# Optimization experiments

Hardware: AMD Instinct MI355X
Metric: run time of the kernel (lower is better)

The kernel has to match this reference:

```python
import jax, jax.numpy as jnp
import numpy as np

N_COARSE = 262145   # GMGN self.n
K_LEVELS = 5        # self.k
M_NBR = 9           # self.m
HID = 2048          # hidden_channels


def _build_grid():
    # replicates GMGN.init_toep_kernel (mtype='toep_mg')
    n_fine = 2 * (N_COARSE - 1) + 1          # 524289
    x = np.linspace(-1.0, 1.0, n_fine)
    x_lst, idx_lst = [], []
    for _ in range(K_LEVELS):
        n = x.shape[0]
        idx = np.arange((n - 1) // 2 - M_NBR + 1, (n - 1) // 2 + M_NBR)[1::2]  # m-1 center pts
        idx_lst.append(idx)
        x_lst.append(x[idx])
        x = x[::2]                            # injection1d
    x_lst.append(x)                           # coarse grid
    xs = np.concatenate(x_lst)[:, None].astype(np.float32)   # (N_eval, 1)
    nbrs = np.stack(idx_lst[::-1]).astype(np.int64)          # (k, m-1), coarse->fine
    return xs, nbrs


def setup_inputs() -> dict:
    key = jax.random.key(0)
    xs_np, nbrs_np = _build_grid()
    dims = [1, HID, HID, HID, HID, 1]
    inp = {"xs": jnp.asarray(xs_np), "nbrs": jnp.asarray(nbrs_np), "k": K_LEVELS, "m": M_NBR}
    ks = jax.random.split(key, 10)
    for j in range(5):
        bd = 1.0 / np.sqrt(dims[j])           # nn.Linear default init range
        inp[f"w{j}"] = jax.random.uniform(ks[2 * j], (dims[j], dims[j + 1]), jnp.float32, -bd, bd)
        inp[f"b{j}"] = jax.random.uniform(ks[2 * j + 1], (dims[j + 1],), jnp.float32, -bd, bd)
    return inp


def _interp1d(a):
    # linear prolongation: (n,) -> (2n-1,); even slots copy, odd slots average
    out = jnp.zeros((2 * a.shape[0] - 1,), a.dtype)
    out = out.at[0::2].set(a)
    return out.at[1::2].set(0.5 * (a[:-1] + a[1:]))


def _forward(xs, Ws, bs, nbrs, k, m):
    h = xs
    for W, b in zip(Ws, bs):
        h = jax.nn.relu(h @ W + b)            # MLP appends relu after every Linear (incl. last)
    Amg = h[:, 0]                             # (N_eval,) pointwise kernel values
    band = m - 1
    Abands = [Amg[band * i: band * (i + 1)] for i in range(k)][::-1]
    Ah = Amg[band * k:]                       # coarse kernel, length (n0-1)/2^k + 1
    for i in range(k):
        Ah = _interp1d(Ah)                    # upsample one level
        Ah = Ah.at[nbrs[i]].set(Abands[i])    # overwrite center band with exact MLP evals
    return Ah[None, None]                     # (1, 1, 2*(n-1)+1)


def reference(xs, w0, b0, w1, b1, w2, b2, w3, b3, w4, b4, nbrs, k, m):
    return _forward(xs, (w0, w1, w2, w3, w4), (b0, b1, b2, b3, b4), nbrs, k, m)
```

## Files before the change

kernel.cpp:

```cpp
#include <hip/hip_runtime.h>
#include <stdint.h>

#define HID    2048
#define MPTS   16425
#define MTILES 129
#define NTIL   16
#define KTIL   64
#define BIMG   5120

typedef float    f32x4 __attribute__((ext_vector_type(4)));
typedef _Float16 f16x8 __attribute__((ext_vector_type(8)));


__global__ void pack_w16(const float* __restrict__ w1,
                         const float* __restrict__ w2,
                         const float* __restrict__ w3,
                         _Float16* __restrict__ wp) {
    const int kt = blockIdx.x, nt = blockIdx.y, L = blockIdx.z;
    const float* W = (L == 0) ? w1 : ((L == 1) ? w2 : w3);
    __shared__ float tl[128 * 33];
    const int tid = threadIdx.x;
    const int k  = tid >> 3;
    const int nc = (tid & 7) * 16;
    const float* src = W + (size_t)(kt * 32 + k) * HID + nt * 128 + nc;
    #pragma unroll
    for (int j = 0; j < 16; ++j) tl[(nc + j) * 33 + k] = src[j];
    __syncthreads();
    const size_t base = (size_t)(L * 1024 + nt * 64 + kt) * BIMG;
    for (int e = tid; e < BIMG; e += 256) {
        int n = e / 40, kk = e - n * 40;
        wp[base + e] = (kk < 32) ? (_Float16)tl[n * 33 + kk] : (_Float16)0.f;
    }
}

__global__ void layer0p(const float* __restrict__ xs,
                        const float* __restrict__ w0,
                        const float* __restrict__ b0,
                        _Float16* __restrict__ Ahg,
                        _Float16* __restrict__ Alg, int row0) {
    const int r = blockIdx.x;
    const int grow = row0 + r;
    const int j0 = threadIdx.x * 8;
    const float x = (grow < MPTS) ? xs[grow] : 0.f;
    f16x8 h, l;
    #pragma unroll
    for (int q = 0; q < 8; ++q) {
        float v = x * w0[j0 + q] + b0[j0 + q];
        v = v > 0.f ? v : 0.f;
        _Float16 hs = (_Float16)v;
        h[q] = hs;
        l[q] = (_Float16)(v - (float)hs);
    }
    const int t = r >> 7, rowgrp = (r >> 4) & 7, lidx = r & 15;
    const int kt = j0 >> 5, quad = (j0 >> 3) & 3;
    const size_t dst = ((size_t)(t * 64 + kt) << 12) + rowgrp * 512 + quad * 128 + lidx * 8;
    *(f16x8*)(Ahg + dst) = h;
    *(f16x8*)(Alg + dst) = l;
}

__launch_bounds__(256, 3)
__global__ void gemm_hl(const _Float16* __restrict__ Ahg,
                        const _Float16* __restrict__ Alg,
                        const _Float16* __restrict__ wp,
                        const float* __restrict__ bias,
                        _Float16* __restrict__ Chg,
                        _Float16* __restrict__ Clg,
                        int layer, int write_lo) {
    __shared__ _Float16 Bs[4][BIMG];

    const int tid  = threadIdx.x;
    const int lane = tid & 63;
    const int wave = tid >> 6;
    const int quad = lane >> 4;
    const int lidx = lane & 15;

    const int nwg = (int)(gridDim.x * gridDim.y);
    const int L   = (int)(blockIdx.y * gridDim.x + blockIdx.x);
    const int F   = (L & 7) * (nwg >> 3) + (L >> 3);
    const int nt  = F & 15;
    const int mt  = F >> 4;

    const int mbase = (wave >> 1) * 64;
    const int nbase = (wave & 1) * 64;

    const char* gW = (const char*)(wp + (size_t)(layer * 1024 + nt * 64) * BIMG);

    const size_t abase = ((size_t)(mt * 64) << 12) + (size_t)(mbase >> 4) * 512 + (size_t)lane * 8;
    const _Float16* aH = Ahg + abase;
    const _Float16* aL = Alg + abase;

    f32x4 acc[4][4];
    #pragma unroll
    for (int i = 0; i < 4; ++i)
        #pragma unroll
        for (int j = 0; j < 4; ++j) acc[i][j] = (f32x4)0.f;

#define PF_B(KT, BUF) do {                                                            \
    const char* nW_ = gW + (size_t)(KT) * (BIMG * 2);                                 \
    char* dW_ = (char*)&Bs[BUF][0];                                                   \
    for (int t = wave; t < 10; t += 4) {                                              \
        __builtin_amdgcn_global_load_lds(                                             \
            (const __attribute__((address_space(1))) unsigned int*)(nW_ + t * 1024 + lane * 16), \
            (__attribute__((address_space(3))) unsigned int*)(dW_ + t * 1024), 16, 0, 0); \
    }                                                                                 \
} while (0)

#define LD_A(KT, H, Lo) do {                                                          \
    const size_t ak_ = (size_t)(KT) << 12;                                            \
    _Pragma("unroll")                                                                 \
    for (int mm = 0; mm < 4; ++mm) {                                                  \
        H[mm]  = *(const f16x8*)(aH + ak_ + mm * 512);                                \
        Lo[mm] = *(const f16x8*)(aL + ak_ + mm * 512);                                \
    }                                                                                 \
} while (0)

#define LD_B(BUF, BF) do {                                                            \
    _Pragma("unroll")                                                                 \
    for (int nn = 0; nn < 4; ++nn) {                                                  \
        int r_ = nbase + nn * 16 + lidx;                                              \
        BF[nn] = *(const f16x8*)(&Bs[BUF][r_ * 40 + quad * 8]);                       \
    }                                                                                 \
} while (0)

#define MFMA32(AH, AL, BF) do {                                                       \
    _Pragma("unroll")                                                                 \
    for (int mm = 0; mm < 4; ++mm)                                                    \
        _Pragma("unroll")                                                             \
        for (int nn = 0; nn < 4; ++nn) {                                              \
            acc[mm][nn] = __builtin_amdgcn_mfma_f32_16x16x32_f16(AH[mm], BF[nn], acc[mm][nn], 0, 0, 0); \
            acc[mm][nn] = __builtin_amdgcn_mfma_f32_16x16x32_f16(AL[mm], BF[nn], acc[mm][nn], 0, 0, 0); \
        }                                                                             \
} while (0)

#define SUPER(S, P, DO_PF, DO_A2) do {                                                \
    f16x8 bfr0_[4];                                                                   \
    LD_B(2 * (P), bfr0_);                                                             \
    if (DO_PF) { PF_B(2 * (S) + 2, 2 * ((P) ^ 1)); PF_B(2 * (S) + 3, 2 * ((P) ^ 1) + 1); } \
    LD_A(2 * (S) + 1, nah, nal);                                                      \
    MFMA32(cah, cal, bfr0_);                                                          \
    f16x8 bfr1_[4];                                                                   \
    LD_B(2 * (P) + 1, bfr1_);                                                         \
    if (DO_A2) LD_A(2 * (S) + 2, cah, cal);                                           \
    MFMA32(nah, nal, bfr1_);                                                          \
    __syncthreads();                                                                  \
} while (0)

    f16x8 cah[4], cal[4], nah[4], nal[4];

    PF_B(0, 0);
    PF_B(1, 1);
    LD_A(0, cah, cal);
    __syncthreads();

    for (int ss = 0; ss < 15; ++ss) {
        SUPER(2 * ss,     0, 1, 1);
        SUPER(2 * ss + 1, 1, 1, 1);
    }
    SUPER(30, 0, 1, 1);
    SUPER(31, 1, 0, 0);

#undef SUPER
#undef MFMA32
#undef LD_B
#undef LD_A
#undef PF_B

    #pragma unroll
    for (int nn = 0; nn < 4; ++nn) {
        const int col = nt * 128 + nbase + nn * 16 + lidx;
        const float bv = bias[col];
        const int kt2 = col >> 5, quad2 = (col >> 3) & 3, j2 = col & 7;
        const size_t cb = ((size_t)(mt * 64 + kt2) << 12) + quad2 * 128 + j2;
        #pragma unroll
        for (int mm = 0; mm < 4; ++mm) {
            const int rowg = (mbase >> 4) + mm;
            #pragma unroll
            for (int r = 0; r < 4; ++r) {
                const int lidx2 = quad * 4 + r;
                float v = acc[mm][nn][r] + bv;
                v = v > 0.f ? v : 0.f;
                _Float16 hs = (_Float16)v;
                const size_t idx = cb + rowg * 512 + lidx2 * 8;
                Chg[idx] = hs;
                if (write_lo) Clg[idx] = (_Float16)(v - (float)hs);
            }
        }
    }
}

__global__ void layer4p(const _Float16* __restrict__ Ahg,
                        const float* __restrict__ w4,
                        const float* __restrict__ b4,
                        float* __restrict__ Amg, int row0) {
    __shared__ float ps[256];
    const int mt = blockIdx.x;
    const int t = threadIdx.x;
    const int row = t & 127, half = t >> 7;
    const int rowgrp = row >> 4, lidx = row & 15;
    const size_t base = ((size_t)(mt * 64) << 12) + rowgrp * 512 + lidx * 8;
    float s = 0.f;
    for (int kt = half * 32; kt < half * 32 + 32; ++kt) {
        const _Float16* ph = Ahg + base + ((size_t)kt << 12);
        const float* wv = w4 + kt * 32;
        #pragma unroll
        for (int quad = 0; quad < 4; ++quad) {
            f16x8 hv = *(const f16x8*)(ph + quad * 128);
            #pragma unroll
            for (int j = 0; j < 8; ++j)
                s += (float)hv[j] * wv[quad * 8 + j];
        }
    }
    ps[t] = s;
    __syncthreads();
    if (t < 128) {
        const int grow = row0 + mt * 128 + t;
        if (grow < MPTS) {
            float v = ps[t] + ps[t + 128] + b4[0];
            Amg[grow] = v > 0.f ? v : 0.f;
        }
    }
}

__global__ void layer0f(const float* __restrict__ xs, const float* __restrict__ w0,
                        const float* __restrict__ b0, float* __restrict__ A, int row0) {
    const int r = blockIdx.x;
    const int j = threadIdx.x * 8;
    const float x = (row0 + r < MPTS) ? xs[row0 + r] : 0.f;
    float* out = A + (size_t)r * HID + j;
    #pragma unroll
    for (int q = 0; q < 8; ++q) {
        float v = x * w0[j + q] + b0[j + q];
        out[q] = v > 0.f ? v : 0.f;
    }
}

__launch_bounds__(256)
__global__ void gemm_valu(const float* __restrict__ A, const float* __restrict__ W,
                          const float* __restrict__ bias, float* __restrict__ C) {
    __shared__ float As[16][132];
    __shared__ float Ws[16][132];
    const int tid = threadIdx.x;
    const int tx = tid & 15, ty = tid >> 4;
    const int n0 = blockIdx.x * 128;
    const int m0 = blockIdx.y * 128;
    const int am = tid & 127, ak = (tid >> 7) * 8;
    const int wn = (tid & 15) * 8, wk = tid >> 4;
    const float* aptr = A + (size_t)(m0 + am) * HID + ak;
    const float* wptr = W + (size_t)wk * HID + n0 + wn;
    float acc[8][8];
    #pragma unroll
    for (int i = 0; i < 8; ++i)
        #pragma unroll
        for (int j = 0; j < 8; ++j) acc[i][j] = 0.f;
    for (int k0 = 0; k0 < HID; k0 += 16) {
        f32x4 a0 = *(const f32x4*)(aptr + k0);
        f32x4 a1 = *(const f32x4*)(aptr + k0 + 4);
        f32x4 w0v = *(const f32x4*)(wptr + (size_t)k0 * HID);
        f32x4 w1v = *(const f32x4*)(wptr + (size_t)k0 * HID + 4);
        __syncthreads();
        As[ak + 0][am] = a0[0]; As[ak + 1][am] = a0[1];
        As[ak + 2][am] = a0[2]; As[ak + 3][am] = a0[3];
        As[ak + 4][am] = a1[0]; As[ak + 5][am] = a1[1];
        As[ak + 6][am] = a1[2]; As[ak + 7][am] = a1[3];
        *(f32x4*)&Ws[wk][wn]     = w0v;
        *(f32x4*)&Ws[wk][wn + 4] = w1v;
        __syncthreads();
        #pragma unroll
        for (int kk = 0; kk < 16; ++kk) {
            f32x4 av0 = *(const f32x4*)&As[kk][ty * 8];
            f32x4 av1 = *(const f32x4*)&As[kk][ty * 8 + 4];
            f32x4 bv0 = *(const f32x4*)&Ws[kk][tx * 8];
            f32x4 bv1 = *(const f32x4*)&Ws[kk][tx * 8 + 4];
            float a[8] = {av0[0], av0[1], av0[2], av0[3], av1[0], av1[1], av1[2], av1[3]};
            float b[8] = {bv0[0], bv0[1], bv0[2], bv0[3], bv1[0], bv1[1], bv1[2], bv1[3]};
            #pragma unroll
            for (int i = 0; i < 8; ++i)
                #pragma unroll
                for (int j = 0; j < 8; ++j) acc[i][j] += a[i] * b[j];
        }
    }
    #pragma unroll
    for (int i = 0; i < 8; ++i) {
        const int m = m0 + ty * 8 + i;
        #pragma unroll
        for (int jc = 0; jc < 2; ++jc) {
            const int n = n0 + tx * 8 + jc * 4;
            f32x4 v4;
            #pragma unroll
            for (int q = 0; q < 4; ++q) {
                float v = acc[i][jc * 4 + q] + bias[n + q];
                v4[q] = v > 0.f ? v : 0.f;
            }
            *(f32x4*)(C + (size_t)m * HID + n) = v4;
        }
    }
}

__global__ void layer4f(const float* __restrict__ A, const float* __restrict__ w4,
                        const float* __restrict__ b4, float* __restrict__ Amg, int row0) {
    const int lane = threadIdx.x & 63;
    const int wave = threadIdx.x >> 6;
    const int r    = blockIdx.x * 4 + wave;
    if (row0 + r >= MPTS) return;
    const float* ap = A + (size_t)r * HID;
    float s = 0.f;
    #pragma unroll
    for (int c = 0; c < 8; ++c) {
        const int col = c * 256 + lane * 4;
        f32x4 av = *(const f32x4*)(ap + col);
        f32x4 wv = *(const f32x4*)(w4 + col);
        s += av[0] * wv[0] + av[1] * wv[1] + av[2] * wv[2] + av[3] * wv[3];
    }
    #pragma unroll
    for (int off = 32; off; off >>= 1) s += __shfl_down(s, off);
    if (lane == 0) {
        float v = s + b4[0];
        Amg[row0 + r] = v > 0.f ? v : 0.f;
    }
}

__global__ void mg_level(const float* __restrict__ in, float* __restrict__ outf,
                         const int* __restrict__ nbrs_base, int level,
                         const float* __restrict__ band, int n_out) {
    const int j = blockIdx.x * 256 + threadIdx.x;
    if (j >= n_out) return;
    float v;
    if (j & 1) v = 0.5f * (in[j >> 1] + in[(j >> 1) + 1]);
    else       v = in[j >> 1];
    const int stride =
        (nbrs_base[1] == 0 && nbrs_base[3] == 0 && nbrs_base[5] == 0) ? 2 : 1;
    #pragma unroll
    for (int t = 0; t < 8; ++t) {
        const int idx = nbrs_base[(level * 8 + t) * stride];
        if (j == idx) v = band[t];
    }
    outf[j] = v;
}

extern "C" void kernel_launch(void* const* d_in, const int* in_sizes, int n_in,
                              void* d_out, int out_size, void* d_ws, size_t ws_size,
                              hipStream_t stream) {
    int iXS=0, iNB=1, iW0=4, iB0=5, iW1=6, iB1=7, iW2=8, iB2=9,
        iW3=10, iB3=11, iW4=12, iB4=13;
    if (n_in >= 14) {
        if (in_sizes[0] == HID) {
            iB0=0; iB1=1; iB2=2; iB3=3; iB4=4; iNB=7;
            iW0=8; iW1=9; iW2=10; iW3=11; iW4=12; iXS=13;
        } else if (!(in_sizes[1] == 40 || in_sizes[1] == 80)) {
            iXS=0; iW0=1; iB0=2; iW1=3; iB1=4; iW2=5; iB2=6;
            iW3=7; iB3=8; iW4=9; iB4=10; iNB=11;
        }
    }
    const float* xs = (const float*)d_in[iXS];
    const int* nbrs = (const int*)d_in[iNB];
    const float* w0 = (const float*)d_in[iW0];
    const float* b0 = (const float*)d_in[iB0];
    const float* w1 = (const float*)d_in[iW1];
    const float* b1 = (const float*)d_in[iB1];
    const float* w2 = (const float*)d_in[iW2];
    const float* b2 = (const float*)d_in[iB2];
    const float* w3 = (const float*)d_in[iW3];
    const float* b3 = (const float*)d_in[iB3];
    const float* w4 = (const float*)d_in[iW4];
    const float* b4 = (const float*)d_in[iB4];

    char* ws = (char*)d_ws;
    const size_t szAmg = 66048;
    const size_t szAh1 = 524544;
    const size_t szAh2 = 1048832;
    float* Amg = (float*)(ws);
    float* ahA = (float*)(ws + szAmg);
    float* ahB = (float*)(ws + szAmg + szAh1);
    const size_t casc_end = szAmg + szAh1 + szAh2;
    const size_t szW    = (size_t)3 * 1024 * BIMG * 2;
    const size_t per_tile = 2ull * 128 * HID * 4;

    const int use_mfma = (ws_size >= casc_end + szW + per_tile) ? 1 : 0;

    _Float16* wp = (_Float16*)(ws + casc_end);
    const size_t buf_start = use_mfma ? (casc_end + szW) : casc_end;

    size_t avail = ws_size - buf_start;
    int CT = (int)(avail / per_tile);
    if (CT < 1) CT = 1;
    if (CT > 96) CT = 96;

    if (use_mfma) {
        const size_t half = (size_t)CT * 128 * HID;
        _Float16* bAh = (_Float16*)(ws + buf_start);
        _Float16* bAl = bAh + half;
        _Float16* bBh = bAh + 2 * half;
        _Float16* bBl = bAh + 3 * half;

        pack_w16<<<dim3(KTIL, NTIL, 3), 256, 0, stream>>>(w1, w2, w3, wp);

        for (int t0 = 0; t0 < MTILES; t0 += CT) {
            int tiles = (MTILES - t0 < CT) ? (MTILES - t0) : CT;
            int row0 = t0 * 128;
            layer0p<<<dim3(tiles * 128), 256, 0, stream>>>(xs, w0, b0, bAh, bAl, row0);
            dim3 ggrid(NTIL, tiles);
            gemm_hl<<<ggrid, 256, 0, stream>>>(bAh, bAl, wp, b1, bBh, bBl, 0, 1);
            gemm_hl<<<ggrid, 256, 0, stream>>>(bBh, bBl, wp, b2, bAh, bAl, 1, 1);
            gemm_hl<<<ggrid, 256, 0, stream>>>(bAh, bAl, wp, b3, bBh, bBl, 2, 0);
            layer4p<<<dim3(tiles), 256, 0, stream>>>(bBh, w4, b4, Amg, row0);
        }
    } else {
        float* bufA = (float*)(ws + buf_start);
        float* bufB = (float*)(ws + buf_start + (size_t)CT * 128 * HID * 4);
        for (int t0 = 0; t0 < MTILES; t0 += CT) {
            int tiles = (MTILES - t0 < CT) ? (MTILES - t0) : CT;
            int row0 = t0 * 128;
            layer0f<<<dim3(tiles * 128), 256, 0, stream>>>(xs, w0, b0, bufA, row0);
            dim3 ggrid(NTIL, tiles);
            gemm_valu<<<ggrid, 256, 0, stream>>>(bufA, w1, b1, bufB);
            gemm_valu<<<ggrid, 256, 0, stream>>>(bufB, w2, b2, bufA);
            gemm_valu<<<ggrid, 256, 0, stream>>>(bufA, w3, b3, bufB);
            layer4f<<<dim3(tiles * 32), 256, 0, stream>>>(bufB, w4, b4, Amg, row0);
        }
    }

    const float* cur = Amg + 40;
    float* dsts[5] = {ahA, ahB, ahA, ahB, (float*)d_out};
    int n = 16385;
    for (int i = 0; i < 5; ++i) {
        int n_out = 2 * n - 1;
        mg_level<<<dim3((n_out + 255) / 256), 256, 0, stream>>>(
            cur, dsts[i], nbrs, i, Amg + 8 * (4 - i), n_out);
        cur = dsts[i];
        n = n_out;
    }
    (void)out_size;
}
```

Baseline: 1.031 ms.

## Restructure GEMM k-loop into 4-slot ring with vmcnt-gated barriers

Replaces the double-buffered super-iteration loop of the hi/lo fp16 MFMA GEMM with a four-slot LDS ring that prefetches B three k-tiles ahead via global_load_lds. Each step waits only on a counted vmcnt before a raw s_barrier, rather than a full __syncthreads after every pair of tiles. MFMA sections run at raised wave priority. This aims for deeper latency hiding and fewer full drains, at the cost of more LDS per block (which may lower occupancy) and fragile hand-tuned wait counts. Each wave now issues 3 fixed 1 KB chunks, so B reads run past the 10 KB tile; the weight buffer is padded to cover the overrun.

```diff
diff --git a/kernel.cpp b/kernel.cpp
--- a/kernel.cpp
+++ b/kernel.cpp
@@ -7,6 +7,7 @@
 #define NTIL   16
 #define KTIL   64
 #define BIMG   5120
+#define BSLOT  6144
 
 typedef float    f32x4 __attribute__((ext_vector_type(4)));
 typedef _Float16 f16x8 __attribute__((ext_vector_type(8)));
@@ -66,7 +67,7 @@
                         _Float16* __restrict__ Chg,
                         _Float16* __restrict__ Clg,
                         int layer, int write_lo) {
-    __shared__ _Float16 Bs[4][BIMG];
+    __shared__ _Float16 Bs[4][BSLOT];
 
     const int tid  = threadIdx.x;
     const int lane = tid & 63;
@@ -98,10 +99,12 @@
 #define PF_B(KT, BUF) do {                                                            \
     const char* nW_ = gW + (size_t)(KT) * (BIMG * 2);                                 \
     char* dW_ = (char*)&Bs[BUF][0];                                                   \
-    for (int t = wave; t < 10; t += 4) {                                              \
+    const int t0_ = wave * 3;                                                         \
+    _Pragma("unroll")                                                                 \
+    for (int c_ = 0; c_ < 3; ++c_) {                                                  \
         __builtin_amdgcn_global_load_lds(                                             \
-            (const __attribute__((address_space(1))) unsigned int*)(nW_ + t * 1024 + lane * 16), \
-            (__attribute__((address_space(3))) unsigned int*)(dW_ + t * 1024), 16, 0, 0); \
+            (const __attribute__((address_space(1))) unsigned int*)(nW_ + (t0_ + c_) * 1024 + lane * 16), \
+            (__attribute__((address_space(3))) unsigned int*)(dW_ + (t0_ + c_) * 1024), 16, 0, 0); \
     }                                                                                 \
 } while (0)
 
@@ -132,34 +135,48 @@
         }                                                                             \
 } while (0)
 
-#define SUPER(S, P, DO_PF, DO_A2) do {                                                \
-    f16x8 bfr0_[4];                                                                   \
-    LD_B(2 * (P), bfr0_);                                                             \
-    if (DO_PF) { PF_B(2 * (S) + 2, 2 * ((P) ^ 1)); PF_B(2 * (S) + 3, 2 * ((P) ^ 1) + 1); } \
-    LD_A(2 * (S) + 1, nah, nal);                                                      \
-    MFMA32(cah, cal, bfr0_);                                                          \
-    f16x8 bfr1_[4];                                                                   \
-    LD_B(2 * (P) + 1, bfr1_);                                                         \
-    if (DO_A2) LD_A(2 * (S) + 2, cah, cal);                                           \
-    MFMA32(nah, nal, bfr1_);                                                          \
-    __syncthreads();                                                                  \
+#define GATE(N) do {                                                                  \
+    asm volatile("s_waitcnt vmcnt(%0)" :: "n"(N));                                    \
+    __builtin_amdgcn_sched_barrier(0);                                                \
+    __builtin_amdgcn_s_barrier();                                                     \
+    __builtin_amdgcn_sched_barrier(0);                                                \
+} while (0)
+
+#define BODY(KT, BUF, GN, DO_PF, DO_A, CH, CL, NH, NL) do {                           \
+    GATE(GN);                                                                         \
+    f16x8 bfr_[4];                                                                    \
+    LD_B(BUF, bfr_);                                                                  \
+    if (DO_A)  LD_A((KT) + 1, NH, NL);                                                \
+    if (DO_PF) PF_B((KT) + 3, ((KT) + 3) & 3);                                        \
+    __builtin_amdgcn_s_setprio(1);                                                    \
+    MFMA32(CH, CL, bfr_);                                                             \
+    __builtin_amdgcn_s_setprio(0);                                                    \
 } while (0)
 
     f16x8 cah[4], cal[4], nah[4], nal[4];
 
+    LD_A(0, cah, cal);
     PF_B(0, 0);
     PF_B(1, 1);
-    LD_A(0, cah, cal);
-    __syncthreads();
-
-    for (int ss = 0; ss < 15; ++ss) {
-        SUPER(2 * ss,     0, 1, 1);
-        SUPER(2 * ss + 1, 1, 1, 1);
-    }
-    SUPER(30, 0, 1, 1);
-    SUPER(31, 1, 0, 0);
-
-#undef SUPER
+    PF_B(2, 2);
+
+    BODY(0, 0,  6, 1, 1, cah, cal, nah, nal);
+    BODY(1, 1, 14, 1, 1, nah, nal, cah, cal);
+    BODY(2, 2, 22, 1, 1, cah, cal, nah, nal);
+    BODY(3, 3, 22, 1, 1, nah, nal, cah, cal);
+    for (int k4 = 1; k4 < 15; ++k4) {
+        BODY(4 * k4 + 0, 0, 22, 1, 1, cah, cal, nah, nal);
+        BODY(4 * k4 + 1, 1, 22, 1, 1, nah, nal, cah, cal);
+        BODY(4 * k4 + 2, 2, 22, 1, 1, cah, cal, nah, nal);
+        BODY(4 * k4 + 3, 3, 22, 1, 1, nah, nal, cah, cal);
+    }
+    BODY(60, 0, 22, 1, 1, cah, cal, nah, nal);
+    BODY(61, 1, 22, 0, 1, nah, nal, cah, cal);
+    BODY(62, 2, 19, 0, 1, cah, cal, nah, nal);
+    BODY(63, 3, 16, 0, 0, nah, nal, cah, cal);
+
+#undef BODY
+#undef GATE
 #undef MFMA32
 #undef LD_B
 #undef LD_A
@@ -372,7 +389,7 @@
     float* ahA = (float*)(ws + szAmg);
     float* ahB = (float*)(ws + szAmg + szAh1);
     const size_t casc_end = szAmg + szAh1 + szAh2;
-    const size_t szW    = (size_t)3 * 1024 * BIMG * 2;
+    const size_t szW    = (size_t)3 * 1024 * BIMG * 2 + 4096;
     const size_t per_tile = 2ull * 128 * HID * 4;
 
     const int use_mfma = (ws_size >= casc_end + szW + per_tile) ? 1 : 0;
```

Result: slower. 1.300 ms (+26.1%).

## Fuse final linear layer into third GEMM epilogue and relax barrier wait

Applied to the files above, without the earlier changes.

The last 2048->1 layer is folded into the third GEMM's epilogue. Each wave computes relu(acc+bias)*w4 partial sums, reduces them with shuffles, and atomically accumulates them into a zeroed Amg buffer. The final bias and relu are applied later inside the first multigrid level kernel, so the layer-3 activations no longer need to be written out or re-read by a separate kernel. The per-superstep __syncthreads is also replaced with a partial vmcnt(8) wait plus a raw barrier to keep prefetch loads in flight. In exchange this adds float atomics, which make summation order nondeterministic, and depends on the waitcnt count being correct.

```diff
diff --git a/kernel.cpp b/kernel.cpp
--- a/kernel.cpp
+++ b/kernel.cpp
@@ -65,7 +65,9 @@
                         const float* __restrict__ bias,
                         _Float16* __restrict__ Chg,
                         _Float16* __restrict__ Clg,
-                        int layer, int write_lo) {
+                        int layer, int write_lo,
+                        float* __restrict__ Amg4,
+                        const float* __restrict__ w4g, int row0) {
     __shared__ _Float16 Bs[4][BIMG];
 
     const int tid  = threadIdx.x;
@@ -130,6 +132,13 @@
             acc[mm][nn] = __builtin_amdgcn_mfma_f32_16x16x32_f16(AH[mm], BF[nn], acc[mm][nn], 0, 0, 0); \
             acc[mm][nn] = __builtin_amdgcn_mfma_f32_16x16x32_f16(AL[mm], BF[nn], acc[mm][nn], 0, 0, 0); \
         }                                                                             \
+} while (0)
+
+#define GATE8() do {                                                                  \
+    asm volatile("s_waitcnt vmcnt(8)" ::: "memory");                                  \
+    __builtin_amdgcn_sched_barrier(0);                                                \
+    __builtin_amdgcn_s_barrier();                                                     \
+    __builtin_amdgcn_sched_barrier(0);                                                \
 } while (0)
 
 #define SUPER(S, P, DO_PF, DO_A2) do {                                                \
@@ -142,7 +151,7 @@
     LD_B(2 * (P) + 1, bfr1_);                                                         \
     if (DO_A2) LD_A(2 * (S) + 2, cah, cal);                                           \
     MFMA32(nah, nal, bfr1_);                                                          \
-    __syncthreads();                                                                  \
+    GATE8();                                                                          \
 } while (0)
 
     f16x8 cah[4], cal[4], nah[4], nal[4];
@@ -160,10 +169,42 @@
     SUPER(31, 1, 0, 0);
 
 #undef SUPER
+#undef GATE8
 #undef MFMA32
 #undef LD_B
 #undef LD_A
 #undef PF_B
+
+    if (Amg4) {
+        float w4v[4], bv[4];
+        #pragma unroll
+        for (int nn = 0; nn < 4; ++nn) {
+            const int col = nt * 128 + nbase + nn * 16 + lidx;
+            w4v[nn] = w4g[col];
+            bv[nn]  = bias[col];
+        }
+        #pragma unroll
+        for (int mm = 0; mm < 4; ++mm) {
+            #pragma unroll
+            for (int r = 0; r < 4; ++r) {
+                float p = 0.f;
+                #pragma unroll
+                for (int nn = 0; nn < 4; ++nn) {
+                    float v = acc[mm][nn][r] + bv[nn];
+                    v = v > 0.f ? v : 0.f;
+                    p += v * w4v[nn];
+                }
+                #pragma unroll
+                for (int off = 1; off <= 8; off <<= 1)
+                    p += __shfl_xor(p, off, 16);
+                if (lidx == 0) {
+                    const int grow = row0 + mt * 128 + mbase + mm * 16 + quad * 4 + r;
+                    if (grow < MPTS) atomicAdd(Amg4 + grow, p);
+                }
+            }
+        }
+        return;
+    }
 
     #pragma unroll
     for (int nn = 0; nn < 4; ++nn) {
@@ -184,39 +225,6 @@
                 Chg[idx] = hs;
                 if (write_lo) Clg[idx] = (_Float16)(v - (float)hs);
             }
-        }
-    }
-}
-
-__global__ void layer4p(const _Float16* __restrict__ Ahg,
-                        const float* __restrict__ w4,
-                        const float* __restrict__ b4,
-                        float* __restrict__ Amg, int row0) {
-    __shared__ float ps[256];
-    const int mt = blockIdx.x;
-    const int t = threadIdx.x;
-    const int row = t & 127, half = t >> 7;
-    const int rowgrp = row >> 4, lidx = row & 15;
-    const size_t base = ((size_t)(mt * 64) << 12) + rowgrp * 512 + lidx * 8;
-    float s = 0.f;
-    for (int kt = half * 32; kt < half * 32 + 32; ++kt) {
-        const _Float16* ph = Ahg + base + ((size_t)kt << 12);
-        const float* wv = w4 + kt * 32;
-        #pragma unroll
-        for (int quad = 0; quad < 4; ++quad) {
-            f16x8 hv = *(const f16x8*)(ph + quad * 128);
-            #pragma unroll
-            for (int j = 0; j < 8; ++j)
-                s += (float)hv[j] * wv[quad * 8 + j];
-        }
-    }
-    ps[t] = s;
-    __syncthreads();
-    if (t < 128) {
-        const int grow = row0 + mt * 128 + t;
-        if (grow < MPTS) {
-            float v = ps[t] + ps[t + 128] + b4[0];
-            Amg[grow] = v > 0.f ? v : 0.f;
         }
     }
 }
@@ -321,18 +329,31 @@
 
 __global__ void mg_level(const float* __restrict__ in, float* __restrict__ outf,
                          const int* __restrict__ nbrs_base, int level,
-                         const float* __restrict__ band, int n_out) {
+                         const float* __restrict__ band, int n_out,
+                         const float* __restrict__ b4p, int xin) {
     const int j = blockIdx.x * 256 + threadIdx.x;
     if (j >= n_out) return;
+    const float b4v = b4p ? b4p[0] : 0.f;
     float v;
-    if (j & 1) v = 0.5f * (in[j >> 1] + in[(j >> 1) + 1]);
-    else       v = in[j >> 1];
+    if (j & 1) {
+        float a = in[j >> 1], b = in[(j >> 1) + 1];
+        if (xin) { a = fmaxf(a + b4v, 0.f); b = fmaxf(b + b4v, 0.f); }
+        v = 0.5f * (a + b);
+    } else {
+        float a = in[j >> 1];
+        if (xin) a = fmaxf(a + b4v, 0.f);
+        v = a;
+    }
     const int stride =
         (nbrs_base[1] == 0 && nbrs_base[3] == 0 && nbrs_base[5] == 0) ? 2 : 1;
     #pragma unroll
     for (int t = 0; t < 8; ++t) {
         const int idx = nbrs_base[(level * 8 + t) * stride];
-        if (j == idx) v = band[t];
+        if (j == idx) {
+            float bb = band[t];
+            if (b4p) bb = fmaxf(bb + b4v, 0.f);
+            v = bb;
+        }
     }
     outf[j] = v;
 }
@@ -392,6 +413,8 @@
         _Float16* bBh = bAh + 2 * half;
         _Float16* bBl = bAh + 3 * half;
 
+        hipMemsetAsync(Amg, 0, (size_t)MPTS * sizeof(float), stream);
+
         pack_w16<<<dim3(KTIL, NTIL, 3), 256, 0, stream>>>(w1, w2, w3, wp);
 
         for (int t0 = 0; t0 < MTILES; t0 += CT) {
@@ -399,10 +422,12 @@
             int row0 = t0 * 128;
             layer0p<<<dim3(tiles * 128), 256, 0, stream>>>(xs, w0, b0, bAh, bAl, row0);
             dim3 ggrid(NTIL, tiles);
-            gemm_hl<<<ggrid, 256, 0, stream>>>(bAh, bAl, wp, b1, bBh, bBl, 0, 1);
-            gemm_hl<<<ggrid, 256, 0, stream>>>(bBh, bBl, wp, b2, bAh, bAl, 1, 1);
-            gemm_hl<<<ggrid, 256, 0, stream>>>(bAh, bAl, wp, b3, bBh, bBl, 2, 0);
-            layer4p<<<dim3(tiles), 256, 0, stream>>>(bBh, w4, b4, Amg, row0);
+            gemm_hl<<<ggrid, 256, 0, stream>>>(bAh, bAl, wp, b1, bBh, bBl, 0, 1,
+                                               nullptr, nullptr, 0);
+            gemm_hl<<<ggrid, 256, 0, stream>>>(bBh, bBl, wp, b2, bAh, bAl, 1, 1,
+                                               nullptr, nullptr, 0);
+            gemm_hl<<<ggrid, 256, 0, stream>>>(bAh, bAl, wp, b3, bBh, bBl, 2, 0,
+                                               Amg, w4, row0);
         }
     } else {
         float* bufA = (float*)(ws + buf_start);
@@ -419,13 +444,15 @@
         }
     }
 
+    const float* b4p = use_mfma ? b4 : nullptr;
     const float* cur = Amg + 40;
     float* dsts[5] = {ahA, ahB, ahA, ahB, (float*)d_out};
     int n = 16385;
     for (int i = 0; i < 5; ++i) {
         int n_out = 2 * n - 1;
         mg_level<<<dim3((n_out + 255) / 256), 256, 0, stream>>>(
-            cur, dsts[i], nbrs, i, Amg + 8 * (4 - i), n_out);
+            cur, dsts[i], nbrs, i, Amg + 8 * (4 - i), n_out,
+            b4p, (i == 0 && use_mfma) ? 1 : 0);
         cur = dsts[i];
         n = n_out;
     }
```

After: 1.006 ms. 1.03x faster.
